# Performance work log

Hardware: AMD Instinct MI355X
Metric: run time of the kernel (lower is better)

The kernel has to match this reference:

```python
import jax, jax.numpy as jnp
import numpy as np

B, S, D, H = 2, 2048, 1024, 16
DK = D // H


def setup_inputs() -> dict:
    key = jax.random.key(0)
    ks = jax.random.split(key, 8)
    Q = jax.random.normal(ks[0], (B, S, D), dtype=jnp.float32)
    K = jax.random.normal(ks[1], (B, S, D), dtype=jnp.float32)
    V = jax.random.normal(ks[2], (B, S, D), dtype=jnp.float32)
    # causal mask (1 = keep), broadcastable to [B, H, S, S]
    mask = jnp.tril(jnp.ones((S, S), dtype=bool))[None, None, :, :]
    # xavier_uniform for [D, D]: bound = sqrt(6 / (D + D))
    bound = float(np.sqrt(6.0 / (D + D)))
    def xavier(k):
        return jax.random.uniform(k, (D, D), jnp.float32, -bound, bound)
    Wq, Wk, Wv, Wo = xavier(ks[3]), xavier(ks[4]), xavier(ks[5]), xavier(ks[6])
    bq = jnp.zeros((D,), jnp.float32)
    bk = jnp.zeros((D,), jnp.float32)
    bv = jnp.zeros((D,), jnp.float32)
    bo = jnp.zeros((D,), jnp.float32)
    return {"Q": Q, "K": K, "V": V, "mask": mask,
            "Wq": Wq, "bq": bq, "Wk": Wk, "bk": bk,
            "Wv": Wv, "bv": bv, "Wo": Wo, "bo": bo}


def _split_heads(x):
    # [B, S, D] -> [B, H, S, DK]
    b, s, _ = x.shape
    return x.reshape(b, s, H, DK).transpose(0, 2, 1, 3)


def reference(Q, K, V, mask, Wq, bq, Wk, bk, Wv, bv, Wo, bo):
    # linear projections (torch Linear: x @ W.T + b)
    q = _split_heads(Q @ Wq.T + bq)  # [B, H, S, DK]
    k = _split_heads(K @ Wk.T + bk)
    v = _split_heads(V @ Wv.T + bv)
    scale = 1.0 / jnp.sqrt(jnp.asarray(DK, q.dtype))
    scores = jnp.einsum('bhqd,bhkd->bhqk', q, k) * scale  # [B, H, S, S]
    scores = jnp.where(mask, scores, jnp.asarray(-1e9, scores.dtype))
    attn = jax.nn.softmax(scores, axis=-1)
    ctx = jnp.einsum('bhqk,bhkd->bhqd', attn, v)  # [B, H, S, DK]
    ctx = ctx.transpose(0, 2, 1, 3).reshape(Q.shape[0], Q.shape[1], D)
    out = ctx @ Wo.T + bo  # dropout is identity in eval mode
    return out, attn
```

## Files before the change

kernel.cpp:

```cpp
#include <hip/hip_runtime.h>
#include <hip/hip_bf16.h>

#define B_  2
#define S_  2048
#define D_  1024
#define H_  16
#define DK_ 64
#define M_  (B_*S_)

typedef __attribute__((ext_vector_type(8))) short short8;
typedef __attribute__((ext_vector_type(4))) float f32x4;

static __device__ __forceinline__ unsigned short f2bf(float f) {
    union { float f; unsigned u; } v; v.f = f;
    unsigned r = (v.u + 0x7fffu + ((v.u >> 16) & 1u)) >> 16;
    return (unsigned short)r;
}

__global__ __launch_bounds__(256) void gemm_mfma(const void* __restrict__ Xv,
                                                 const float* __restrict__ W,
                                                 const float* __restrict__ bias,
                                                 void* __restrict__ outv,
                                                 int a_bf16, int out_mode)
{
    __shared__ unsigned short as_[128][40];
    __shared__ unsigned short bs_[128][40];

    const int tid  = threadIdx.x;
    const int wave = tid >> 6, lane = tid & 63;
    const int lq   = lane & 15, quad = lane >> 4;
    const int m0   = blockIdx.y * 128, n0 = blockIdx.x * 128;
    const int wm   = (wave >> 1) * 64, wn = (wave & 1) * 64;

    f32x4 acc[4][4] = {};

    for (int k0 = 0; k0 < D_; k0 += 32) {
        __syncthreads();
        if (a_bf16) {
            const unsigned short* X = (const unsigned short*)Xv;
            #pragma unroll
            for (int i = 0; i < 2; ++i) {
                int idx = tid + i*256;
                int row = idx >> 2, c = idx & 3;
                *(short8*)&as_[row][c*8] =
                    *(const short8*)(X + (size_t)(m0+row)*D_ + k0 + c*8);
            }
        } else {
            const float* X = (const float*)Xv;
            #pragma unroll
            for (int i = 0; i < 4; ++i) {
                int idx = tid + i*256;
                int row = idx >> 3, c = idx & 7;
                float4 v = *(const float4*)(X + (size_t)(m0+row)*D_ + k0 + c*4);
                union { unsigned short u[4]; unsigned long long ll; } cv;
                cv.u[0]=f2bf(v.x); cv.u[1]=f2bf(v.y); cv.u[2]=f2bf(v.z); cv.u[3]=f2bf(v.w);
                *(unsigned long long*)&as_[row][c*4] = cv.ll;
            }
        }
        #pragma unroll
        for (int i = 0; i < 4; ++i) {
            int idx = tid + i*256;
            int row = idx >> 3, c = idx & 7;
            float4 v = *(const float4*)(W + (size_t)(n0+row)*D_ + k0 + c*4);
            union { unsigned short u[4]; unsigned long long ll; } cv;
            cv.u[0]=f2bf(v.x); cv.u[1]=f2bf(v.y); cv.u[2]=f2bf(v.z); cv.u[3]=f2bf(v.w);
            *(unsigned long long*)&bs_[row][c*4] = cv.ll;
        }
        __syncthreads();

        short8 a[4], b[4];
        #pragma unroll
        for (int i = 0; i < 4; ++i) a[i] = *(const short8*)&as_[wm + i*16 + lq][quad*8];
        #pragma unroll
        for (int j = 0; j < 4; ++j) b[j] = *(const short8*)&bs_[wn + j*16 + lq][quad*8];
        #pragma unroll
        for (int i = 0; i < 4; ++i)
            #pragma unroll
            for (int j = 0; j < 4; ++j)
                acc[i][j] = __builtin_amdgcn_mfma_f32_16x16x32_bf16(a[i], b[j], acc[i][j], 0, 0, 0);
    }

    float bcol[4];
    #pragma unroll
    for (int j = 0; j < 4; ++j) bcol[j] = bias[n0 + wn + j*16 + lq];

    if (out_mode == 0) {
        float* out = (float*)outv;
        #pragma unroll
        for (int i = 0; i < 4; ++i)
            #pragma unroll
            for (int j = 0; j < 4; ++j) {
                const int col = n0 + wn + j*16 + lq;
                #pragma unroll
                for (int r = 0; r < 4; ++r) {
                    const int m = m0 + wm + i*16 + quad*4 + r;
                    out[(size_t)m*D_ + col] = acc[i][j][r] + bcol[j];
                }
            }
    } else {
        unsigned short* out = (unsigned short*)outv;
        #pragma unroll
        for (int i = 0; i < 4; ++i)
            #pragma unroll
            for (int j = 0; j < 4; ++j) {
                const int col = n0 + wn + j*16 + lq;
                const int h = col >> 6, dk = col & 63;
                #pragma unroll
                for (int r = 0; r < 4; ++r) {
                    const int m  = m0 + wm + i*16 + quad*4 + r;
                    const int bb = m >> 11, s = m & (S_-1);
                    out[(((size_t)(bb*H_ + h))*S_ + s)*DK_ + dk] = f2bf(acc[i][j][r] + bcol[j]);
                }
            }
    }
}

__global__ __launch_bounds__(256) void transpose_v(const unsigned short* __restrict__ vp,
                                                   unsigned short* __restrict__ vt)
{
    __shared__ unsigned short ts[64][72];
    const int tid = threadIdx.x;
    const int s0  = blockIdx.x * 64;
    const size_t bh = (size_t)blockIdx.z * H_ + blockIdx.y;
    const unsigned short* src = vp + (bh * S_ + s0) * DK_;
    #pragma unroll
    for (int i = 0; i < 2; ++i) {
        int idx = tid + i*256;
        *(short8*)&ts[idx >> 3][(idx & 7)*8] = *(const short8*)(src + idx*8);
    }
    __syncthreads();
    unsigned short* dst = vt + bh * DK_ * S_;
    #pragma unroll
    for (int i = 0; i < 2; ++i) {
        int idx = tid + i*256;
        int dk = idx >> 3, c = idx & 7;
        union { unsigned short u[8]; short8 v; } pk;
        #pragma unroll
        for (int j = 0; j < 8; ++j) pk.u[j] = ts[c*8 + j][dk];
        *(short8*)(dst + (size_t)dk*S_ + s0 + c*8) = pk.v;
    }
}

__global__ __launch_bounds__(256) void attn_mfma(const unsigned short* __restrict__ q,
                                                 const unsigned short* __restrict__ k,
                                                 const unsigned short* __restrict__ vt,
                                                 float* __restrict__ attn,
                                                 unsigned short* __restrict__ ctx)
{
    __shared__ unsigned short qs[64][72];
    __shared__ unsigned short ks[64][72];
    __shared__ unsigned short vts[64][72];
    __shared__ unsigned short es[4][16][72];

    const int tid  = threadIdx.x;
    const int wave = tid >> 6, lane = tid & 63;
    const int lq   = lane & 15, quad = lane >> 4;
    const int it = blockIdx.x, h = blockIdx.y, b = blockIdx.z;
    const size_t bh = (size_t)(b*H_ + h);
    const unsigned short* qb  = q  + (bh*S_ + (size_t)it*64) * DK_;
    const unsigned short* kb  = k  + bh*S_*DK_;
    const unsigned short* vtb = vt + bh*DK_*S_;
    float* attn_b = attn + bh*(size_t)S_*S_ + (size_t)it*64*S_;

    #pragma unroll
    for (int i = 0; i < 2; ++i) {
        int idx = tid + i*256;
        *(short8*)&qs[idx >> 3][(idx & 7)*8] = *(const short8*)(qb + idx*8);
    }

    const int wr0 = wave*16;
    const int rg0 = it*64 + wr0 + quad*4;

    float rsum[4] = {0.f, 0.f, 0.f, 0.f};
    for (int jt = 0; jt <= it; ++jt) {
        __syncthreads();
        #pragma unroll
        for (int i = 0; i < 2; ++i) {
            int idx = tid + i*256;
            *(short8*)&ks[idx >> 3][(idx & 7)*8] =
                *(const short8*)(kb + (size_t)jt*64*DK_ + idx*8);
        }
        __syncthreads();
        const short8 a0 = *(const short8*)&qs[wr0 + lq][quad*8];
        const short8 a1 = *(const short8*)&qs[wr0 + lq][32 + quad*8];
        #pragma unroll
        for (int j = 0; j < 4; ++j) {
            f32x4 sacc = {};
            sacc = __builtin_amdgcn_mfma_f32_16x16x32_bf16(
                a0, *(const short8*)&ks[j*16 + lq][quad*8], sacc, 0, 0, 0);
            sacc = __builtin_amdgcn_mfma_f32_16x16x32_bf16(
                a1, *(const short8*)&ks[j*16 + lq][32 + quad*8], sacc, 0, 0, 0);
            const int cg = jt*64 + j*16 + lq;
            #pragma unroll
            for (int r = 0; r < 4; ++r)
                if (cg <= rg0 + r) rsum[r] += __expf(sacc[r]*0.125f);
        }
    }
    #pragma unroll
    for (int m = 1; m < 16; m <<= 1)
        #pragma unroll
        for (int r = 0; r < 4; ++r)
            rsum[r] += __shfl_xor(rsum[r], m, 64);
    float inv_r[4];
    #pragma unroll
    for (int r = 0; r < 4; ++r) inv_r[r] = 1.0f / rsum[r];

    f32x4 cacc[4] = {};
    for (int jt = 0; jt <= it; ++jt) {
        __syncthreads();
        #pragma unroll
        for (int i = 0; i < 2; ++i) {
            int idx = tid + i*256;
            int row = idx >> 3, c = idx & 7;
            *(short8*)&ks[row][c*8] = *(const short8*)(kb + (size_t)jt*64*DK_ + idx*8);
            *(short8*)&vts[row][c*8] = *(const short8*)(vtb + (size_t)row*S_ + jt*64 + c*8);
        }
        __syncthreads();
        const short8 a0 = *(const short8*)&qs[wr0 + lq][quad*8];
        const short8 a1 = *(const short8*)&qs[wr0 + lq][32 + quad*8];
        #pragma unroll
        for (int j = 0; j < 4; ++j) {
            f32x4 sacc = {};
            sacc = __builtin_amdgcn_mfma_f32_16x16x32_bf16(
                a0, *(const short8*)&ks[j*16 + lq][quad*8], sacc, 0, 0, 0);
            sacc = __builtin_amdgcn_mfma_f32_16x16x32_bf16(
                a1, *(const short8*)&ks[j*16 + lq][32 + quad*8], sacc, 0, 0, 0);
            const int cg = jt*64 + j*16 + lq;
            #pragma unroll
            for (int r = 0; r < 4; ++r) {
                const float e = (cg <= rg0 + r) ? __expf(sacc[r]*0.125f)*inv_r[r] : 0.f;
                attn_b[(size_t)(wr0 + quad*4 + r)*S_ + cg] = e;
                es[wave][quad*4 + r][j*16 + lq] = f2bf(e);
            }
        }
        const short8 p0 = *(const short8*)&es[wave][lq][quad*8];
        const short8 p1 = *(const short8*)&es[wave][lq][32 + quad*8];
        #pragma unroll
        for (int j = 0; j < 4; ++j) {
            cacc[j] = __builtin_amdgcn_mfma_f32_16x16x32_bf16(
                p0, *(const short8*)&vts[j*16 + lq][quad*8], cacc[j], 0, 0, 0);
            cacc[j] = __builtin_amdgcn_mfma_f32_16x16x32_bf16(
                p1, *(const short8*)&vts[j*16 + lq][32 + quad*8], cacc[j], 0, 0, 0);
        }
    }

    #pragma unroll
    for (int j = 0; j < 4; ++j) {
        const int dk = j*16 + lq;
        #pragma unroll
        for (int r = 0; r < 4; ++r) {
            const int srow = it*64 + wr0 + quad*4 + r;
            ctx[((size_t)b*S_ + srow)*D_ + h*DK_ + dk] = f2bf(cacc[j][r]);
        }
    }

    const int zc0 = (it+1)*64;
    if (zc0 < S_) {
        const float4 z4 = make_float4(0.f, 0.f, 0.f, 0.f);
        float* rowp = attn_b + (size_t)(tid >> 2)*S_;
        for (int c = zc0 + (tid & 3)*4; c < S_; c += 16)
            *(float4*)&rowp[c] = z4;
    }
}

extern "C" void kernel_launch(void* const* d_in, const int* in_sizes, int n_in,
                              void* d_out, int out_size, void* d_ws, size_t ws_size,
                              hipStream_t stream)
{
    const float* Q  = (const float*)d_in[0];
    const float* K  = (const float*)d_in[1];
    const float* V  = (const float*)d_in[2];
    const float* Wq = (const float*)d_in[4];
    const float* bq = (const float*)d_in[5];
    const float* Wk = (const float*)d_in[6];
    const float* bk = (const float*)d_in[7];
    const float* Wv = (const float*)d_in[8];
    const float* bv = (const float*)d_in[9];
    const float* Wo = (const float*)d_in[10];
    const float* bo = (const float*)d_in[11];

    float* out  = (float*)d_out;
    float* attn = out + (size_t)B_*S_*D_;
    unsigned short* ws = (unsigned short*)d_ws;
    const size_t R = (size_t)B_*S_*D_;
    unsigned short* qp  = ws;
    unsigned short* kp  = ws + R;
    unsigned short* vp  = ws + 2*R;
    unsigned short* vtw = ws + 3*R;
    unsigned short* ctx = ws + 4*R;

    dim3 ggrid(D_/128, M_/128);
    gemm_mfma<<<ggrid, 256, 0, stream>>>(Q, Wq, bq, qp, 0, 1);
    gemm_mfma<<<ggrid, 256, 0, stream>>>(K, Wk, bk, kp, 0, 1);
    gemm_mfma<<<ggrid, 256, 0, stream>>>(V, Wv, bv, vp, 0, 1);
    transpose_v<<<dim3(S_/64, H_, B_), 256, 0, stream>>>(vp, vtw);
    attn_mfma<<<dim3(S_/64, H_, B_), 256, 0, stream>>>(qp, kp, vtw, attn, ctx);
    gemm_mfma<<<ggrid, 256, 0, stream>>>(ctx, Wo, bo, out, 1, 0);
}
```

Before: 994.3 us.

## Pre-convert inputs to bf16, use LDS-direct swizzled GEMM, pair causal attention tiles

A single pass now converts the fp32 inputs and weights to bf16 in workspace. The GEMM is rewritten to load tiles with global_load_lds into an XOR-swizzled shared layout, using 128x64 tiles and a K-step of 64. The attention kernel now has each block handle a short and a long causal query tile (it and NT-1-it) to balance work, with XCD-aware block mapping and swizzled shared memory. The aim is to cut redundant fp32 conversion, LDS bank conflicts and causal load imbalance, at the cost of an extra conversion pass and more workspace.

```diff
diff --git a/kernel.cpp b/kernel.cpp
--- a/kernel.cpp
+++ b/kernel.cpp
@@ -7,6 +7,9 @@
 #define H_  16
 #define DK_ 64
 #define M_  (B_*S_)
+#define NT_ (S_/64)
+#define NE_ (B_*S_*D_)
+#define NW_ (D_*D_)
 
 typedef __attribute__((ext_vector_type(8))) short short8;
 typedef __attribute__((ext_vector_type(4))) float f32x4;
@@ -17,79 +20,95 @@
     return (unsigned short)r;
 }
 
-__global__ __launch_bounds__(256) void gemm_mfma(const void* __restrict__ Xv,
-                                                 const float* __restrict__ W,
-                                                 const float* __restrict__ bias,
-                                                 void* __restrict__ outv,
-                                                 int a_bf16, int out_mode)
+static __device__ __forceinline__ void gload16(const void* g, void* l) {
+    __builtin_amdgcn_global_load_lds((const __attribute__((address_space(1))) void*)g,
+                                     (__attribute__((address_space(3))) void*)l, 16, 0, 0);
+}
+
+__global__ __launch_bounds__(256) void conv7(const float* __restrict__ q,  const float* __restrict__ k,
+                                             const float* __restrict__ v,  const float* __restrict__ wq,
+                                             const float* __restrict__ wk, const float* __restrict__ wv,
+                                             const float* __restrict__ wo, unsigned short* __restrict__ ws)
 {
-    __shared__ unsigned short as_[128][40];
-    __shared__ unsigned short bs_[128][40];
+    const float* src[7] = {q, k, v, wq, wk, wv, wo};
+    const int    n4[7]  = {NE_/4, NE_/4, NE_/4, NW_/4, NW_/4, NW_/4, NW_/4};
+    size_t off = 0;
+    #pragma unroll
+    for (int seg = 0; seg < 7; ++seg) {
+        unsigned short* dst = ws + off;
+        for (int i = blockIdx.x*256 + threadIdx.x; i < n4[seg]; i += gridDim.x*256) {
+            float4 x = ((const float4*)src[seg])[i];
+            union { unsigned short u[4]; unsigned long long ll; } cv;
+            cv.u[0]=f2bf(x.x); cv.u[1]=f2bf(x.y); cv.u[2]=f2bf(x.z); cv.u[3]=f2bf(x.w);
+            ((unsigned long long*)dst)[i] = cv.ll;
+        }
+        off += (size_t)n4[seg]*4;
+    }
+}
+
+__global__ __launch_bounds__(256) void gemm_bt(const unsigned short* __restrict__ A,
+                                               const unsigned short* __restrict__ Bt,
+                                               const float* __restrict__ bias,
+                                               void* __restrict__ outv, int out_mode)
+{
+    __shared__ unsigned short as_[128][64];
+    __shared__ unsigned short bs_[64][64];
 
     const int tid  = threadIdx.x;
     const int wave = tid >> 6, lane = tid & 63;
     const int lq   = lane & 15, quad = lane >> 4;
-    const int m0   = blockIdx.y * 128, n0 = blockIdx.x * 128;
-    const int wm   = (wave >> 1) * 64, wn = (wave & 1) * 64;
-
-    f32x4 acc[4][4] = {};
-
-    for (int k0 = 0; k0 < D_; k0 += 32) {
-        __syncthreads();
-        if (a_bf16) {
-            const unsigned short* X = (const unsigned short*)Xv;
-            #pragma unroll
-            for (int i = 0; i < 2; ++i) {
-                int idx = tid + i*256;
-                int row = idx >> 2, c = idx & 3;
-                *(short8*)&as_[row][c*8] =
-                    *(const short8*)(X + (size_t)(m0+row)*D_ + k0 + c*8);
-            }
-        } else {
-            const float* X = (const float*)Xv;
+    const int m0   = blockIdx.y * 128, n0 = blockIdx.x * 64;
+    const int wm   = (wave >> 1) * 64, wn = (wave & 1) * 32;
+
+    f32x4 acc[4][2] = {};
+
+    for (int k0 = 0; k0 < D_; k0 += 64) {
+        __syncthreads();
+        #pragma unroll
+        for (int i = 0; i < 4; ++i) {
+            const int p = tid + i*256, row = p >> 3, c = (p & 7) ^ (row & 7);
+            gload16(A + (size_t)(m0+row)*D_ + k0 + c*8,
+                    (char*)as_ + (size_t)(wave*64 + i*256)*16);
+        }
+        #pragma unroll
+        for (int i = 0; i < 2; ++i) {
+            const int p = tid + i*256, row = p >> 3, c = (p & 7) ^ (row & 7);
+            gload16(Bt + (size_t)(n0+row)*D_ + k0 + c*8,
+                    (char*)bs_ + (size_t)(wave*64 + i*256)*16);
+        }
+        __syncthreads();
+
+        #pragma unroll
+        for (int kk = 0; kk < 2; ++kk) {
+            short8 a[4], b[2];
             #pragma unroll
             for (int i = 0; i < 4; ++i) {
-                int idx = tid + i*256;
-                int row = idx >> 3, c = idx & 7;
-                float4 v = *(const float4*)(X + (size_t)(m0+row)*D_ + k0 + c*4);
-                union { unsigned short u[4]; unsigned long long ll; } cv;
-                cv.u[0]=f2bf(v.x); cv.u[1]=f2bf(v.y); cv.u[2]=f2bf(v.z); cv.u[3]=f2bf(v.w);
-                *(unsigned long long*)&as_[row][c*4] = cv.ll;
-            }
-        }
-        #pragma unroll
-        for (int i = 0; i < 4; ++i) {
-            int idx = tid + i*256;
-            int row = idx >> 3, c = idx & 7;
-            float4 v = *(const float4*)(W + (size_t)(n0+row)*D_ + k0 + c*4);
-            union { unsigned short u[4]; unsigned long long ll; } cv;
-            cv.u[0]=f2bf(v.x); cv.u[1]=f2bf(v.y); cv.u[2]=f2bf(v.z); cv.u[3]=f2bf(v.w);
-            *(unsigned long long*)&bs_[row][c*4] = cv.ll;
-        }
-        __syncthreads();
-
-        short8 a[4], b[4];
-        #pragma unroll
-        for (int i = 0; i < 4; ++i) a[i] = *(const short8*)&as_[wm + i*16 + lq][quad*8];
-        #pragma unroll
-        for (int j = 0; j < 4; ++j) b[j] = *(const short8*)&bs_[wn + j*16 + lq][quad*8];
-        #pragma unroll
-        for (int i = 0; i < 4; ++i)
-            #pragma unroll
-            for (int j = 0; j < 4; ++j)
-                acc[i][j] = __builtin_amdgcn_mfma_f32_16x16x32_bf16(a[i], b[j], acc[i][j], 0, 0, 0);
-    }
-
-    float bcol[4];
-    #pragma unroll
-    for (int j = 0; j < 4; ++j) bcol[j] = bias[n0 + wn + j*16 + lq];
+                const int row = wm + i*16 + lq;
+                a[i] = *(const short8*)((const char*)as_ + row*128 + (((kk*4+quad) ^ (row&7))*16));
+            }
+            #pragma unroll
+            for (int j = 0; j < 2; ++j) {
+                const int row = wn + j*16 + lq;
+                b[j] = *(const short8*)((const char*)bs_ + row*128 + (((kk*4+quad) ^ (row&7))*16));
+            }
+            #pragma unroll
+            for (int i = 0; i < 4; ++i)
+                #pragma unroll
+                for (int j = 0; j < 2; ++j)
+                    acc[i][j] = __builtin_amdgcn_mfma_f32_16x16x32_bf16(a[i], b[j], acc[i][j], 0, 0, 0);
+        }
+    }
+
+    float bcol[2];
+    #pragma unroll
+    for (int j = 0; j < 2; ++j) bcol[j] = bias[n0 + wn + j*16 + lq];
 
     if (out_mode == 0) {
         float* out = (float*)outv;
         #pragma unroll
         for (int i = 0; i < 4; ++i)
             #pragma unroll
-            for (int j = 0; j < 4; ++j) {
+            for (int j = 0; j < 2; ++j) {
                 const int col = n0 + wn + j*16 + lq;
                 #pragma unroll
                 for (int r = 0; r < 4; ++r) {
@@ -102,7 +121,7 @@
         #pragma unroll
         for (int i = 0; i < 4; ++i)
             #pragma unroll
-            for (int j = 0; j < 4; ++j) {
+            for (int j = 0; j < 2; ++j) {
                 const int col = n0 + wn + j*16 + lq;
                 const int h = col >> 6, dk = col & 63;
                 #pragma unroll
@@ -147,100 +166,183 @@
                                                  float* __restrict__ attn,
                                                  unsigned short* __restrict__ ctx)
 {
-    __shared__ unsigned short qs[64][72];
-    __shared__ unsigned short ks[64][72];
-    __shared__ unsigned short vts[64][72];
+    __shared__ unsigned short qs[2][64][64];
+    __shared__ unsigned short ks[64][64];
+    __shared__ unsigned short vts[64][64];
     __shared__ unsigned short es[4][16][72];
 
     const int tid  = threadIdx.x;
     const int wave = tid >> 6, lane = tid & 63;
     const int lq   = lane & 15, quad = lane >> 4;
-    const int it = blockIdx.x, h = blockIdx.y, b = blockIdx.z;
+
+    const int g = blockIdx.x;
+    const int xcd = g & 7, i5 = g >> 3;
+    const int x = i5 >> 2;
+    const int bhid = xcd + 8*(i5 & 3);
+    const int h = bhid & (H_-1), b = bhid >> 4;
+
+    const int itA = x, itB = NT_-1 - x;
     const size_t bh = (size_t)(b*H_ + h);
-    const unsigned short* qb  = q  + (bh*S_ + (size_t)it*64) * DK_;
     const unsigned short* kb  = k  + bh*S_*DK_;
-    const unsigned short* vtb = vt + bh*DK_*S_;
-    float* attn_b = attn + bh*(size_t)S_*S_ + (size_t)it*64*S_;
-
-    #pragma unroll
-    for (int i = 0; i < 2; ++i) {
-        int idx = tid + i*256;
-        *(short8*)&qs[idx >> 3][(idx & 7)*8] = *(const short8*)(qb + idx*8);
-    }
-
-    const int wr0 = wave*16;
-    const int rg0 = it*64 + wr0 + quad*4;
-
-    float rsum[4] = {0.f, 0.f, 0.f, 0.f};
-    for (int jt = 0; jt <= it; ++jt) {
-        __syncthreads();
+    const unsigned short* vtb = vt + bh*(size_t)DK_*S_;
+    const unsigned short* qbA = q + (bh*S_ + (size_t)itA*64) * DK_;
+    const unsigned short* qbB = q + (bh*S_ + (size_t)itB*64) * DK_;
+    float* attn_bA = attn + bh*(size_t)S_*S_ + (size_t)itA*64*S_;
+    float* attn_bB = attn + bh*(size_t)S_*S_ + (size_t)itB*64*S_;
+
+    #pragma unroll
+    for (int t = 0; t < 2; ++t) {
+        const unsigned short* qb = t ? qbB : qbA;
         #pragma unroll
         for (int i = 0; i < 2; ++i) {
-            int idx = tid + i*256;
-            *(short8*)&ks[idx >> 3][(idx & 7)*8] =
-                *(const short8*)(kb + (size_t)jt*64*DK_ + idx*8);
-        }
-        __syncthreads();
-        const short8 a0 = *(const short8*)&qs[wr0 + lq][quad*8];
-        const short8 a1 = *(const short8*)&qs[wr0 + lq][32 + quad*8];
+            const int p = tid + i*256, row = p >> 3, c = (p & 7) ^ (row & 7);
+            gload16(qb + (size_t)row*DK_ + c*8,
+                    (char*)&qs[t][0][0] + (size_t)(wave*64 + i*256)*16);
+        }
+    }
+    __syncthreads();
+
+    const int wr0  = wave*16;
+    const int rgA0 = itA*64 + wr0 + quad*4;
+    const int rgB0 = itB*64 + wr0 + quad*4;
+
+    short8 aA0, aA1, aB0, aB1;
+    {
+        const int row = wr0 + lq;
+        const int s0 = ((quad)     ^ (row & 7)) * 16;
+        const int s1 = ((4 + quad) ^ (row & 7)) * 16;
+        aA0 = *(const short8*)((const char*)&qs[0][row][0] + s0);
+        aA1 = *(const short8*)((const char*)&qs[0][row][0] + s1);
+        aB0 = *(const short8*)((const char*)&qs[1][row][0] + s0);
+        aB1 = *(const short8*)((const char*)&qs[1][row][0] + s1);
+    }
+
+    float rsA[4] = {0.f,0.f,0.f,0.f}, rsB[4] = {0.f,0.f,0.f,0.f};
+    for (int jt = 0; jt <= itB; ++jt) {
+        __syncthreads();
+        #pragma unroll
+        for (int i = 0; i < 2; ++i) {
+            const int p = tid + i*256, row = p >> 3, c = (p & 7) ^ (row & 7);
+            gload16(kb + ((size_t)jt*64 + row)*DK_ + c*8,
+                    (char*)&ks[0][0] + (size_t)(wave*64 + i*256)*16);
+        }
+        __syncthreads();
+        const int actA = (jt <= itA);
         #pragma unroll
         for (int j = 0; j < 4; ++j) {
-            f32x4 sacc = {};
-            sacc = __builtin_amdgcn_mfma_f32_16x16x32_bf16(
-                a0, *(const short8*)&ks[j*16 + lq][quad*8], sacc, 0, 0, 0);
-            sacc = __builtin_amdgcn_mfma_f32_16x16x32_bf16(
-                a1, *(const short8*)&ks[j*16 + lq][32 + quad*8], sacc, 0, 0, 0);
+            const int krow = j*16 + lq;
+            const int s0 = ((quad)     ^ (krow & 7)) * 16;
+            const int s1 = ((4 + quad) ^ (krow & 7)) * 16;
+            const short8 b0 = *(const short8*)((const char*)&ks[krow][0] + s0);
+            const short8 b1 = *(const short8*)((const char*)&ks[krow][0] + s1);
             const int cg = jt*64 + j*16 + lq;
-            #pragma unroll
-            for (int r = 0; r < 4; ++r)
-                if (cg <= rg0 + r) rsum[r] += __expf(sacc[r]*0.125f);
+            {
+                f32x4 s = {};
+                s = __builtin_amdgcn_mfma_f32_16x16x32_bf16(aB0, b0, s, 0, 0, 0);
+                s = __builtin_amdgcn_mfma_f32_16x16x32_bf16(aB1, b1, s, 0, 0, 0);
+                #pragma unroll
+                for (int r = 0; r < 4; ++r)
+                    if (cg <= rgB0 + r) rsB[r] += __expf(s[r]*0.125f);
+            }
+            if (actA) {
+                f32x4 s = {};
+                s = __builtin_amdgcn_mfma_f32_16x16x32_bf16(aA0, b0, s, 0, 0, 0);
+                s = __builtin_amdgcn_mfma_f32_16x16x32_bf16(aA1, b1, s, 0, 0, 0);
+                #pragma unroll
+                for (int r = 0; r < 4; ++r)
+                    if (cg <= rgA0 + r) rsA[r] += __expf(s[r]*0.125f);
+            }
         }
     }
     #pragma unroll
     for (int m = 1; m < 16; m <<= 1)
         #pragma unroll
-        for (int r = 0; r < 4; ++r)
-            rsum[r] += __shfl_xor(rsum[r], m, 64);
-    float inv_r[4];
-    #pragma unroll
-    for (int r = 0; r < 4; ++r) inv_r[r] = 1.0f / rsum[r];
-
-    f32x4 cacc[4] = {};
-    for (int jt = 0; jt <= it; ++jt) {
+        for (int r = 0; r < 4; ++r) {
+            rsA[r] += __shfl_xor(rsA[r], m, 64);
+            rsB[r] += __shfl_xor(rsB[r], m, 64);
+        }
+    float invA[4], invB[4];
+    #pragma unroll
+    for (int r = 0; r < 4; ++r) { invA[r] = 1.0f/rsA[r]; invB[r] = 1.0f/rsB[r]; }
+
+    f32x4 cA[4] = {}, cB[4] = {};
+    for (int jt = 0; jt <= itB; ++jt) {
         __syncthreads();
         #pragma unroll
         for (int i = 0; i < 2; ++i) {
-            int idx = tid + i*256;
-            int row = idx >> 3, c = idx & 7;
-            *(short8*)&ks[row][c*8] = *(const short8*)(kb + (size_t)jt*64*DK_ + idx*8);
-            *(short8*)&vts[row][c*8] = *(const short8*)(vtb + (size_t)row*S_ + jt*64 + c*8);
-        }
-        __syncthreads();
-        const short8 a0 = *(const short8*)&qs[wr0 + lq][quad*8];
-        const short8 a1 = *(const short8*)&qs[wr0 + lq][32 + quad*8];
+            const int p = tid + i*256, row = p >> 3, c = (p & 7) ^ (row & 7);
+            gload16(kb + ((size_t)jt*64 + row)*DK_ + c*8,
+                    (char*)&ks[0][0]  + (size_t)(wave*64 + i*256)*16);
+            gload16(vtb + (size_t)row*S_ + jt*64 + c*8,
+                    (char*)&vts[0][0] + (size_t)(wave*64 + i*256)*16);
+        }
+        __syncthreads();
+        const int actA = (jt <= itA);
+
         #pragma unroll
         for (int j = 0; j < 4; ++j) {
-            f32x4 sacc = {};
-            sacc = __builtin_amdgcn_mfma_f32_16x16x32_bf16(
-                a0, *(const short8*)&ks[j*16 + lq][quad*8], sacc, 0, 0, 0);
-            sacc = __builtin_amdgcn_mfma_f32_16x16x32_bf16(
-                a1, *(const short8*)&ks[j*16 + lq][32 + quad*8], sacc, 0, 0, 0);
+            const int krow = j*16 + lq;
+            const int s0 = ((quad)     ^ (krow & 7)) * 16;
+            const int s1 = ((4 + quad) ^ (krow & 7)) * 16;
+            const short8 b0 = *(const short8*)((const char*)&ks[krow][0] + s0);
+            const short8 b1 = *(const short8*)((const char*)&ks[krow][0] + s1);
             const int cg = jt*64 + j*16 + lq;
+            f32x4 s = {};
+            s = __builtin_amdgcn_mfma_f32_16x16x32_bf16(aB0, b0, s, 0, 0, 0);
+            s = __builtin_amdgcn_mfma_f32_16x16x32_bf16(aB1, b1, s, 0, 0, 0);
             #pragma unroll
             for (int r = 0; r < 4; ++r) {
-                const float e = (cg <= rg0 + r) ? __expf(sacc[r]*0.125f)*inv_r[r] : 0.f;
-                attn_b[(size_t)(wr0 + quad*4 + r)*S_ + cg] = e;
+                const float e = (cg <= rgB0 + r) ? __expf(s[r]*0.125f)*invB[r] : 0.f;
+                attn_bB[(size_t)(wr0 + quad*4 + r)*S_ + cg] = e;
                 es[wave][quad*4 + r][j*16 + lq] = f2bf(e);
             }
         }
-        const short8 p0 = *(const short8*)&es[wave][lq][quad*8];
-        const short8 p1 = *(const short8*)&es[wave][lq][32 + quad*8];
-        #pragma unroll
-        for (int j = 0; j < 4; ++j) {
-            cacc[j] = __builtin_amdgcn_mfma_f32_16x16x32_bf16(
-                p0, *(const short8*)&vts[j*16 + lq][quad*8], cacc[j], 0, 0, 0);
-            cacc[j] = __builtin_amdgcn_mfma_f32_16x16x32_bf16(
-                p1, *(const short8*)&vts[j*16 + lq][32 + quad*8], cacc[j], 0, 0, 0);
+        {
+            const short8 p0 = *(const short8*)&es[wave][lq][quad*8];
+            const short8 p1 = *(const short8*)&es[wave][lq][32 + quad*8];
+            #pragma unroll
+            for (int j = 0; j < 4; ++j) {
+                const int vrow = j*16 + lq;
+                const int s0 = ((quad)     ^ (vrow & 7)) * 16;
+                const int s1 = ((4 + quad) ^ (vrow & 7)) * 16;
+                cB[j] = __builtin_amdgcn_mfma_f32_16x16x32_bf16(
+                    p0, *(const short8*)((const char*)&vts[vrow][0] + s0), cB[j], 0, 0, 0);
+                cB[j] = __builtin_amdgcn_mfma_f32_16x16x32_bf16(
+                    p1, *(const short8*)((const char*)&vts[vrow][0] + s1), cB[j], 0, 0, 0);
+            }
+        }
+
+        if (actA) {
+            #pragma unroll
+            for (int j = 0; j < 4; ++j) {
+                const int krow = j*16 + lq;
+                const int s0 = ((quad)     ^ (krow & 7)) * 16;
+                const int s1 = ((4 + quad) ^ (krow & 7)) * 16;
+                const short8 b0 = *(const short8*)((const char*)&ks[krow][0] + s0);
+                const short8 b1 = *(const short8*)((const char*)&ks[krow][0] + s1);
+                const int cg = jt*64 + j*16 + lq;
+                f32x4 s = {};
+                s = __builtin_amdgcn_mfma_f32_16x16x32_bf16(aA0, b0, s, 0, 0, 0);
+                s = __builtin_amdgcn_mfma_f32_16x16x32_bf16(aA1, b1, s, 0, 0, 0);
+                #pragma unroll
+                for (int r = 0; r < 4; ++r) {
+                    const float e = (cg <= rgA0 + r) ? __expf(s[r]*0.125f)*invA[r] : 0.f;
+                    attn_bA[(size_t)(wr0 + quad*4 + r)*S_ + cg] = e;
+                    es[wave][quad*4 + r][j*16 + lq] = f2bf(e);
+                }
+            }
+            const short8 p0 = *(const short8*)&es[wave][lq][quad*8];
+            const short8 p1 = *(const short8*)&es[wave][lq][32 + quad*8];
+            #pragma unroll
+            for (int j = 0; j < 4; ++j) {
+                const int vrow = j*16 + lq;
+                const int s0 = ((quad)     ^ (vrow & 7)) * 16;
+                const int s1 = ((4 + quad) ^ (vrow & 7)) * 16;
+                cA[j] = __builtin_amdgcn_mfma_f32_16x16x32_bf16(
+                    p0, *(const short8*)((const char*)&vts[vrow][0] + s0), cA[j], 0, 0, 0);
+                cA[j] = __builtin_amdgcn_mfma_f32_16x16x32_bf16(
+                    p1, *(const short8*)((const char*)&vts[vrow][0] + s1), cA[j], 0, 0, 0);
+            }
         }
     }
 
@@ -249,17 +351,25 @@
         const int dk = j*16 + lq;
         #pragma unroll
         for (int r = 0; r < 4; ++r) {
-            const int srow = it*64 + wr0 + quad*4 + r;
-            ctx[((size_t)b*S_ + srow)*D_ + h*DK_ + dk] = f2bf(cacc[j][r]);
-        }
-    }
-
-    const int zc0 = (it+1)*64;
-    if (zc0 < S_) {
-        const float4 z4 = make_float4(0.f, 0.f, 0.f, 0.f);
-        float* rowp = attn_b + (size_t)(tid >> 2)*S_;
-        for (int c = zc0 + (tid & 3)*4; c < S_; c += 16)
-            *(float4*)&rowp[c] = z4;
+            const int sA = itA*64 + wr0 + quad*4 + r;
+            const int sB = itB*64 + wr0 + quad*4 + r;
+            ctx[((size_t)b*S_ + sA)*D_ + h*DK_ + dk] = f2bf(cA[j][r]);
+            ctx[((size_t)b*S_ + sB)*D_ + h*DK_ + dk] = f2bf(cB[j][r]);
+        }
+    }
+
+    const float4 z4 = make_float4(0.f, 0.f, 0.f, 0.f);
+    {
+        const int zc0 = (itA+1)*64;
+        float* rowp = attn_bA + (size_t)(tid >> 2)*S_;
+        for (int c = zc0 + (tid & 3)*4; c < S_; c += 16) *(float4*)&rowp[c] = z4;
+    }
+    {
+        const int zc0 = (itB+1)*64;
+        if (zc0 < S_) {
+            float* rowp = attn_bB + (size_t)(tid >> 2)*S_;
+            for (int c = zc0 + (tid & 3)*4; c < S_; c += 16) *(float4*)&rowp[c] = z4;
+        }
     }
 }
 
@@ -281,19 +391,30 @@
 
     float* out  = (float*)d_out;
     float* attn = out + (size_t)B_*S_*D_;
+
     unsigned short* ws = (unsigned short*)d_ws;
-    const size_t R = (size_t)B_*S_*D_;
-    unsigned short* qp  = ws;
-    unsigned short* kp  = ws + R;
-    unsigned short* vp  = ws + 2*R;
-    unsigned short* vtw = ws + 3*R;
-    unsigned short* ctx = ws + 4*R;
-
-    dim3 ggrid(D_/128, M_/128);
-    gemm_mfma<<<ggrid, 256, 0, stream>>>(Q, Wq, bq, qp, 0, 1);
-    gemm_mfma<<<ggrid, 256, 0, stream>>>(K, Wk, bk, kp, 0, 1);
-    gemm_mfma<<<ggrid, 256, 0, stream>>>(V, Wv, bv, vp, 0, 1);
+    const size_t R  = (size_t)NE_;
+    const size_t W1 = (size_t)NW_;
+    unsigned short* Qb  = ws;
+    unsigned short* Kb  = ws + R;
+    unsigned short* Vb  = ws + 2*R;
+    unsigned short* Wqb = ws + 3*R;
+    unsigned short* Wkb = Wqb + W1;
+    unsigned short* Wvb = Wkb + W1;
+    unsigned short* Wob = Wvb + W1;
+    unsigned short* qp  = Wob + W1;
+    unsigned short* kp  = qp + R;
+    unsigned short* vp  = kp + R;
+    unsigned short* vtw = vp + R;
+    unsigned short* ctx = vtw + R;
+
+    conv7<<<2048, 256, 0, stream>>>(Q, K, V, Wq, Wk, Wv, Wo, ws);
+
+    dim3 ggrid(D_/64, M_/128);
+    gemm_bt<<<ggrid, 256, 0, stream>>>(Qb, Wqb, bq, qp, 1);
+    gemm_bt<<<ggrid, 256, 0, stream>>>(Kb, Wkb, bk, kp, 1);
+    gemm_bt<<<ggrid, 256, 0, stream>>>(Vb, Wvb, bv, vp, 1);
     transpose_v<<<dim3(S_/64, H_, B_), 256, 0, stream>>>(vp, vtw);
-    attn_mfma<<<dim3(S_/64, H_, B_), 256, 0, stream>>>(qp, kp, vtw, attn, ctx);
-    gemm_mfma<<<ggrid, 256, 0, stream>>>(ctx, Wo, bo, out, 1, 0);
-}
+    attn_mfma<<<(NT_/2)*H_*B_, 256, 0, stream>>>(qp, kp, vtw, attn, ctx);
+    gemm_bt<<<ggrid, 256, 0, stream>>>(ctx, Wob, bo, out, 0);
+}
```

Measured after the change: 806.2 us. -18.9%, faster.
